# Optimization experiments

Measured on AMD Instinct MI355X. Metric: run time of the kernel, lower is better.

Reference implementation:

```python
import jax, jax.numpy as jnp
import numpy as np
import math

B, S, D, HD = 8, 2048, 768, 64  # batch, seq, emb_hidden_dim, head_dim


def setup_inputs() -> dict:
    key = jax.random.key(0)
    ks = jax.random.split(key, 7)
    scale_w = 1.0 / math.sqrt(D)
    return {
        "X": jax.random.normal(ks[0], (B, S, D), dtype=jnp.float32),
        "Wq": jax.random.normal(ks[1], (D, HD), dtype=jnp.float32) * scale_w,
        "bq": jax.random.normal(ks[2], (HD,), dtype=jnp.float32) * 0.01,
        "Wk": jax.random.normal(ks[3], (D, HD), dtype=jnp.float32) * scale_w,
        "bk": jax.random.normal(ks[4], (HD,), dtype=jnp.float32) * 0.01,
        "Wv": jax.random.normal(ks[5], (D, HD), dtype=jnp.float32) * scale_w,
        "bv": jax.random.normal(ks[6], (HD,), dtype=jnp.float32) * 0.01,
    }


def reference(X, Wq, bq, Wk, bk, Wv, bv):
    # Projections: [B,S,D] @ [D,HD] -> [B,S,HD]
    Q = X @ Wq + bq
    K = X @ Wk + bk
    V = X @ Wv + bv
    # NOTE: original divides by sqrt(hidden_dim)=sqrt(D), not sqrt(head_dim)
    inv_scale = 1.0 / math.sqrt(D)
    scores = jnp.einsum("bqd,bkd->bqk", Q, K) * inv_scale  # [B,S,S]
    causal = jnp.tril(jnp.ones((S, S), dtype=bool))
    scores = jnp.where(causal, scores, -jnp.inf)
    attn = jax.nn.softmax(scores, axis=-1)
    # dropout p=0.0 (eval/deterministic reference)
    return jnp.einsum("bqk,bkd->bqd", attn, V)  # [B,S,HD]
```

## Files before the change

kernel.cpp:

```cpp
#include <hip/hip_runtime.h>
#include <hip/hip_bf16.h>
#include <math.h>

typedef __attribute__((ext_vector_type(8))) short short8;
typedef __attribute__((ext_vector_type(4))) float f32x4;

#define SS 2048
#define DD 768
#define HDIM 64
#define MM 16384

__device__ __forceinline__ short f2bf(float f) {
    union { float f; unsigned u; } v; v.f = f;
    unsigned r = (v.u + 0x7fffu + ((v.u >> 16) & 1u)) >> 16;
    return (short)r;
}

__device__ __forceinline__ void gl_lds(const void* g, void* l) {
    __builtin_amdgcn_global_load_lds(
        (const __attribute__((address_space(1))) unsigned*)g,
        (__attribute__((address_space(3))) unsigned*)l, 16, 0, 0);
}

__global__ void prep_w(const float* __restrict__ Wq, const float* __restrict__ Wk,
                       const float* __restrict__ Wv, short* __restrict__ Wt) {
    int idx = blockIdx.x * 256 + threadIdx.x;
    int col = idx / DD;
    int k   = idx - col * DD;
    const float* W = (col < 64) ? Wq : (col < 128) ? Wk : Wv;
    int c = col & 63;
    Wt[idx] = f2bf(W[k * HDIM + c]);
}

__global__ __launch_bounds__(512)
void proj_qkv(const float* __restrict__ X, const short* __restrict__ Wt,
              const float* __restrict__ bq, const float* __restrict__ bk,
              const float* __restrict__ bv,
              short* __restrict__ Qg, short* __restrict__ Kg, short* __restrict__ Vt) {
    __shared__ float Xl[2][2048];
    __shared__ short Wl[2][12288];
    const int tid = threadIdx.x;
    const int w = tid >> 6, lane = tid & 63;
    const int lr = lane & 15, lg = lane >> 4;
    const int wr = w >> 2, wc = w & 3;
    const int row0 = blockIdx.x * 32;

    f32x4 acc[3];
    #pragma unroll
    for (int cf = 0; cf < 3; cf++) acc[cf] = (f32x4)0.0f;

    auto stage = [&](int kk, int buf) {
        {
            int o = w * 1024 + lane * 16;
            int row = o >> 8, ch = (o >> 4) & 15;
            const char* src = (const char*)X + (size_t)(row0 + row) * 3072
                              + kk * 256 + ((ch ^ (row & 7)) << 4);
            gl_lds(src, (char*)&Xl[buf][0] + w * 1024);
        }
        #pragma unroll
        for (int s = 0; s < 3; s++) {
            int i = w * 3 + s;
            int o = i * 1024 + lane * 16;
            int col = o >> 7, ch = (o >> 4) & 7;
            const char* src = (const char*)Wt + (size_t)col * 1536
                              + kk * 128 + ((ch ^ (col & 7)) << 4);
            gl_lds(src, (char*)&Wl[buf][0] + i * 1024);
        }
    };

    stage(0, 0);
    __syncthreads();
    int buf = 0;
    for (int kk = 0; kk < 12; kk++) {
        if (kk < 11) stage(kk + 1, buf ^ 1);
        const char* xb = (const char*)&Xl[buf][0];
        const char* wb = (const char*)&Wl[buf][0];
        #pragma unroll
        for (int ksub = 0; ksub < 2; ksub++) {
            int r = wr * 16 + lr;
            int b0 = r * 256 + ksub * 128 + lg * 32;
            f32x4 x0 = *(const f32x4*)(xb + ((b0)      ^ ((r & 7) << 4)));
            f32x4 x1 = *(const f32x4*)(xb + ((b0 + 16) ^ ((r & 7) << 4)));
            short8 a;
            a[0]=f2bf(x0[0]); a[1]=f2bf(x0[1]); a[2]=f2bf(x0[2]); a[3]=f2bf(x0[3]);
            a[4]=f2bf(x1[0]); a[5]=f2bf(x1[1]); a[6]=f2bf(x1[2]); a[7]=f2bf(x1[3]);
            #pragma unroll
            for (int cf = 0; cf < 3; cf++) {
                int col = wc * 48 + cf * 16 + lr;
                short8 bfr = *(const short8*)(wb +
                    ((col * 128 + ksub * 64 + lg * 16) ^ ((col & 7) << 4)));
                acc[cf] = __builtin_amdgcn_mfma_f32_16x16x32_bf16(a, bfr, acc[cf], 0, 0, 0);
            }
        }
        __syncthreads();
        buf ^= 1;
    }

    #pragma unroll
    for (int cf = 0; cf < 3; cf++) {
        int gcol = wc * 48 + cf * 16 + lr;
        int m = gcol >> 6, cc = gcol & 63;
        float bias = (m == 0 ? bq : m == 1 ? bk : bv)[cc];
        #pragma unroll
        for (int i = 0; i < 4; i++) {
            int r = row0 + wr * 16 + lg * 4 + i;
            short o = f2bf(acc[cf][i] + bias);
            if (m == 0)      Qg[(size_t)r * HDIM + cc] = o;
            else if (m == 1) Kg[(size_t)r * HDIM + cc] = o;
            else             Vt[(size_t)cc * MM + r]   = o;
        }
    }
}

__global__ __launch_bounds__(512)
void attn_part(const short* __restrict__ Qg, const short* __restrict__ Kg,
               const short* __restrict__ Vt,
               float* __restrict__ Opart, float* __restrict__ Ml) {
    __shared__ short Kl[2][4096];
    __shared__ short Vl[2][4096];
    __shared__ short Pl[8][1024];
    const int tid = threadIdx.x;
    const int w = tid >> 6, lane = tid & 63;
    const int lr = lane & 15, lg = lane >> 4;
    const int b = blockIdx.y;

    int idx = 39 - (int)blockIdx.x;
    int g = 0;
    while (idx >= 2 * (g + 1) * (g + 2)) g++;
    int rem = idx - 2 * g * (g + 1);
    const int J = g * 4 + rem / (g + 1);
    const int c = rem - (rem / (g + 1)) * (g + 1);
    const int t0 = c * 8;
    const int t1 = min(2 * J + 2, t0 + 8);

    const int q0 = J * 128 + w * 16;
    char* plbase = (char*)&Pl[w][0];

    short8 qf[2];
    qf[0] = *(const short8*)(Qg + ((size_t)b * SS + q0 + lr) * HDIM + lg * 8);
    qf[1] = *(const short8*)(Qg + ((size_t)b * SS + q0 + lr) * HDIM + 32 + lg * 8);

    f32x4 oacc[4];
    #pragma unroll
    for (int d = 0; d < 4; d++) oacc[d] = (f32x4)0.0f;
    float mrow[4] = {-INFINITY, -INFINITY, -INFINITY, -INFINITY};
    float lrow[4] = {0.f, 0.f, 0.f, 0.f};
    const float scl = 0.03608439182435161f;

    auto stage = [&](int t, int buf) {
        const int kv0 = t * 64;
        {
            int o = w * 1024 + lane * 16;
            int row = o >> 7, ch = (o >> 4) & 7;
            const char* src = (const char*)Kg + ((size_t)b * SS + kv0) * 128
                              + row * 128 + ((ch ^ (row & 7)) << 4);
            gl_lds(src, (char*)&Kl[buf][0] + w * 1024);
        }
        {
            int o = w * 1024 + lane * 16;
            int col = o >> 7, ch = (o >> 4) & 7;
            const char* src = (const char*)Vt + (size_t)col * (MM * 2)
                              + ((size_t)b * SS + kv0) * 2 + ((ch ^ (col & 7)) << 4);
            gl_lds(src, (char*)&Vl[buf][0] + w * 1024);
        }
    };

    stage(t0, 0);
    __syncthreads();
    int buf = 0;
    for (int t = t0; t < t1; t++) {
        if (t + 1 < t1) stage(t + 1, buf ^ 1);
        const int kv0 = t * 64;
        const bool active = (kv0 <= q0 + 15);
        if (active) {
            const char* kb = (const char*)&Kl[buf][0];
            f32x4 sacc[4];
            #pragma unroll
            for (int ct = 0; ct < 4; ct++) sacc[ct] = (f32x4)0.0f;
            #pragma unroll
            for (int ct = 0; ct < 4; ct++) {
                int row = ct * 16 + lr;
                short8 k0 = *(const short8*)(kb + ((row * 128 +      lg * 16) ^ ((row & 7) << 4)));
                short8 k1 = *(const short8*)(kb + ((row * 128 + 64 + lg * 16) ^ ((row & 7) << 4)));
                sacc[ct] = __builtin_amdgcn_mfma_f32_16x16x32_bf16(qf[0], k0, sacc[ct], 0, 0, 0);
                sacc[ct] = __builtin_amdgcn_mfma_f32_16x16x32_bf16(qf[1], k1, sacc[ct], 0, 0, 0);
            }

            const bool maskt = (kv0 + 63 > q0);
            float p[4][4];
            float rm[4] = {-1e30f, -1e30f, -1e30f, -1e30f};
            #pragma unroll
            for (int ct = 0; ct < 4; ct++) {
                #pragma unroll
                for (int i = 0; i < 4; i++) {
                    float s = sacc[ct][i] * scl;
                    if (maskt) {
                        int kv = kv0 + ct * 16 + lr;
                        int qr = q0 + lg * 4 + i;
                        if (kv > qr) s = -1e30f;
                    }
                    p[ct][i] = s;
                    rm[i] = fmaxf(rm[i], s);
                }
            }
            #pragma unroll
            for (int i = 0; i < 4; i++) {
                float v = rm[i];
                v = fmaxf(v, __shfl_xor(v, 1));
                v = fmaxf(v, __shfl_xor(v, 2));
                v = fmaxf(v, __shfl_xor(v, 4));
                v = fmaxf(v, __shfl_xor(v, 8));
                rm[i] = v;
            }
            float rs[4];
            #pragma unroll
            for (int i = 0; i < 4; i++) {
                float mn = fmaxf(mrow[i], rm[i]);
                float scale = __expf(mrow[i] - mn);
                mrow[i] = mn;
                lrow[i] *= scale;
                for (int d = 0; d < 4; d++) oacc[d][i] *= scale;
                float sum = 0.f;
                #pragma unroll
                for (int ct = 0; ct < 4; ct++) {
                    float e = __expf(p[ct][i] - mn);
                    p[ct][i] = e;
                    sum += e;
                }
                rs[i] = sum;
            }
            #pragma unroll
            for (int i = 0; i < 4; i++) {
                float v = rs[i];
                v += __shfl_xor(v, 1);
                v += __shfl_xor(v, 2);
                v += __shfl_xor(v, 4);
                v += __shfl_xor(v, 8);
                lrow[i] += v;
            }

            #pragma unroll
            for (int ct = 0; ct < 4; ct++) {
                #pragma unroll
                for (int i = 0; i < 4; i++) {
                    int r = lg * 4 + i;
                    int byteoff = r * 128 + (ct * 16 + lr) * 2;
                    *(short*)(plbase + (byteoff ^ ((r & 7) << 4))) = f2bf(p[ct][i]);
                }
            }

            const char* vb = (const char*)&Vl[buf][0];
            #pragma unroll
            for (int ks = 0; ks < 2; ks++) {
                int byteoff = lr * 128 + ks * 64 + lg * 16;
                short8 pf = *(const short8*)(plbase + (byteoff ^ ((lr & 7) << 4)));
                #pragma unroll
                for (int d = 0; d < 4; d++) {
                    int col = d * 16 + lr;
                    short8 vf = *(const short8*)(vb +
                        ((col * 128 + ks * 64 + lg * 16) ^ ((col & 7) << 4)));
                    oacc[d] = __builtin_amdgcn_mfma_f32_16x16x32_bf16(pf, vf, oacc[d], 0, 0, 0);
                }
            }
        }
        __syncthreads();
        buf ^= 1;
    }

    const int pb = (b * 16 + J) * 4 + c;
    float* op = Opart + (size_t)pb * 8192 + (size_t)(w * 16) * 64;
    #pragma unroll
    for (int d = 0; d < 4; d++)
        #pragma unroll
        for (int i = 0; i < 4; i++)
            op[(lg * 4 + i) * 64 + d * 16 + lr] = oacc[d][i];
    if (lr == 0) {
        float* ml = Ml + (size_t)pb * 256;
        for (int i = 0; i < 4; i++) {
            ml[w * 16 + lg * 4 + i]       = mrow[i];
            ml[128 + w * 16 + lg * 4 + i] = lrow[i];
        }
    }
}

__global__ __launch_bounds__(256)
void attn_comb(const float* __restrict__ Opart, const float* __restrict__ Ml,
               float* __restrict__ out) {
    const int J = blockIdx.x, b = blockIdx.y;
    const int nc = (2 * J + 2 + 7) >> 3;
    const int tid = threadIdx.x;
    const int r = tid >> 1, h = tid & 1;
    const int base = (b * 16 + J) * 4;

    float m = -INFINITY;
    for (int c = 0; c < nc; c++) m = fmaxf(m, Ml[(size_t)(base + c) * 256 + r]);

    float L = 0.f;
    f32x4 acc[8];
    #pragma unroll
    for (int q = 0; q < 8; q++) acc[q] = (f32x4)0.0f;
    for (int c = 0; c < nc; c++) {
        const float* ml = Ml + (size_t)(base + c) * 256;
        float sc = __expf(ml[r] - m);
        L += ml[128 + r] * sc;
        const float* op = Opart + (size_t)(base + c) * 8192 + r * 64 + h * 32;
        #pragma unroll
        for (int q = 0; q < 8; q++)
            acc[q] += *(const f32x4*)(op + q * 4) * sc;
    }
    float inv = 1.0f / L;
    float* o = out + ((size_t)b * SS + J * 128 + r) * HDIM + h * 32;
    #pragma unroll
    for (int q = 0; q < 8; q++) {
        f32x4 v = acc[q] * inv;
        *(f32x4*)(o + q * 4) = v;
    }
}

extern "C" void kernel_launch(void* const* d_in, const int* in_sizes, int n_in,
                              void* d_out, int out_size, void* d_ws, size_t ws_size,
                              hipStream_t stream) {
    const float* X  = (const float*)d_in[0];
    const float* Wq = (const float*)d_in[1];
    const float* bq = (const float*)d_in[2];
    const float* Wk = (const float*)d_in[3];
    const float* bk = (const float*)d_in[4];
    const float* Wv = (const float*)d_in[5];
    const float* bv = (const float*)d_in[6];
    float* out = (float*)d_out;

    char* ws = (char*)d_ws;
    short* Wt = (short*)(ws);
    short* Qg = (short*)(ws + 294912);
    short* Kg = (short*)(ws + 294912 + 2097152);
    short* Vt = (short*)(ws + 294912 + 2 * 2097152);
    size_t opOff = 294912 + 3 * (size_t)2097152;
    float* Op = (float*)(ws + opOff);
    float* Ml = (float*)(ws + opOff + (size_t)512 * 8192 * 4);

    prep_w<<<576, 256, 0, stream>>>(Wq, Wk, Wv, Wt);
    proj_qkv<<<512, 512, 0, stream>>>(X, Wt, bq, bk, bv, Qg, Kg, Vt);
    attn_part<<<dim3(40, 8), 512, 0, stream>>>(Qg, Kg, Vt, Op, Ml);
    attn_comb<<<dim3(16, 8), 256, 0, stream>>>(Op, Ml, out);
}
```

Baseline: 62.36 us.

## Skip masked MFMA sub-tiles, write single-chunk rows directly, store partials in bf16

On diagonal tiles the attention kernel now computes only the 16-column sub-tiles at or below the causal boundary, applies the mask only to the boundary sub-tile, and skips P·V k-steps that are entirely masked. Query blocks J<=3 have a single KV chunk, so they normalize and write the final output directly, and the combine kernel only handles J>=4. Partial outputs are stored as bf16 instead of fp32, halving the partial-buffer traffic at some cost in precision. The goal is to cut wasted matrix work, combine work and memory traffic, at the price of more branching and a small accuracy loss.

```diff
diff --git a/kernel.cpp b/kernel.cpp
--- a/kernel.cpp
+++ b/kernel.cpp
@@ -14,6 +14,11 @@
     union { float f; unsigned u; } v; v.f = f;
     unsigned r = (v.u + 0x7fffu + ((v.u >> 16) & 1u)) >> 16;
     return (short)r;
+}
+__device__ __forceinline__ float bf2f(short s) {
+    union { float f; unsigned u; } v;
+    v.u = ((unsigned)(unsigned short)s) << 16;
+    return v.f;
 }
 
 __device__ __forceinline__ void gl_lds(const void* g, void* l) {
@@ -115,7 +120,8 @@
 __global__ __launch_bounds__(512)
 void attn_part(const short* __restrict__ Qg, const short* __restrict__ Kg,
                const short* __restrict__ Vt,
-               float* __restrict__ Opart, float* __restrict__ Ml) {
+               short* __restrict__ Opart, float* __restrict__ Ml,
+               float* __restrict__ out) {
     __shared__ short Kl[2][4096];
     __shared__ short Vl[2][4096];
     __shared__ short Pl[8][1024];
@@ -128,7 +134,7 @@
     int g = 0;
     while (idx >= 2 * (g + 1) * (g + 2)) g++;
     int rem = idx - 2 * g * (g + 1);
-    const int J = g * 4 + rem / (g + 1);
+    const int J = 4 * g + rem / (g + 1);
     const int c = rem - (rem / (g + 1)) * (g + 1);
     const int t0 = c * 8;
     const int t1 = min(2 * J + 2, t0 + 8);
@@ -171,36 +177,43 @@
     for (int t = t0; t < t1; t++) {
         if (t + 1 < t1) stage(t + 1, buf ^ 1);
         const int kv0 = t * 64;
-        const bool active = (kv0 <= q0 + 15);
-        if (active) {
+        const int delta = q0 - kv0;
+        if (delta >= 0) {
+            const int nct = min(4, (delta >> 4) + 1);
+            const int mct = delta >> 4;
+            const int nks = min(2, (delta >> 5) + 1);
+
             const char* kb = (const char*)&Kl[buf][0];
             f32x4 sacc[4];
             #pragma unroll
-            for (int ct = 0; ct < 4; ct++) sacc[ct] = (f32x4)0.0f;
-            #pragma unroll
             for (int ct = 0; ct < 4; ct++) {
-                int row = ct * 16 + lr;
-                short8 k0 = *(const short8*)(kb + ((row * 128 +      lg * 16) ^ ((row & 7) << 4)));
-                short8 k1 = *(const short8*)(kb + ((row * 128 + 64 + lg * 16) ^ ((row & 7) << 4)));
-                sacc[ct] = __builtin_amdgcn_mfma_f32_16x16x32_bf16(qf[0], k0, sacc[ct], 0, 0, 0);
-                sacc[ct] = __builtin_amdgcn_mfma_f32_16x16x32_bf16(qf[1], k1, sacc[ct], 0, 0, 0);
-            }
-
-            const bool maskt = (kv0 + 63 > q0);
+                if (ct < nct) {
+                    int row = ct * 16 + lr;
+                    short8 k0 = *(const short8*)(kb + ((row * 128 +      lg * 16) ^ ((row & 7) << 4)));
+                    short8 k1 = *(const short8*)(kb + ((row * 128 + 64 + lg * 16) ^ ((row & 7) << 4)));
+                    f32x4 s = (f32x4)0.0f;
+                    s = __builtin_amdgcn_mfma_f32_16x16x32_bf16(qf[0], k0, s, 0, 0, 0);
+                    s = __builtin_amdgcn_mfma_f32_16x16x32_bf16(qf[1], k1, s, 0, 0, 0);
+                    sacc[ct] = s;
+                }
+            }
+
             float p[4][4];
             float rm[4] = {-1e30f, -1e30f, -1e30f, -1e30f};
             #pragma unroll
             for (int ct = 0; ct < 4; ct++) {
-                #pragma unroll
-                for (int i = 0; i < 4; i++) {
-                    float s = sacc[ct][i] * scl;
-                    if (maskt) {
-                        int kv = kv0 + ct * 16 + lr;
-                        int qr = q0 + lg * 4 + i;
-                        if (kv > qr) s = -1e30f;
+                if (ct < nct) {
+                    #pragma unroll
+                    for (int i = 0; i < 4; i++) {
+                        float s = sacc[ct][i] * scl;
+                        if (ct == mct) {
+                            int kv = kv0 + ct * 16 + lr;
+                            int qr = q0 + lg * 4 + i;
+                            if (kv > qr) s = -1e30f;
+                        }
+                        p[ct][i] = s;
+                        rm[i] = fmaxf(rm[i], s);
                     }
-                    p[ct][i] = s;
-                    rm[i] = fmaxf(rm[i], s);
                 }
             }
             #pragma unroll
@@ -223,9 +236,11 @@
                 float sum = 0.f;
                 #pragma unroll
                 for (int ct = 0; ct < 4; ct++) {
-                    float e = __expf(p[ct][i] - mn);
-                    p[ct][i] = e;
-                    sum += e;
+                    if (ct < nct) {
+                        float e = __expf(p[ct][i] - mn);
+                        p[ct][i] = e;
+                        sum += e;
+                    }
                 }
                 rs[i] = sum;
             }
@@ -241,25 +256,30 @@
 
             #pragma unroll
             for (int ct = 0; ct < 4; ct++) {
-                #pragma unroll
-                for (int i = 0; i < 4; i++) {
-                    int r = lg * 4 + i;
-                    int byteoff = r * 128 + (ct * 16 + lr) * 2;
-                    *(short*)(plbase + (byteoff ^ ((r & 7) << 4))) = f2bf(p[ct][i]);
+                if (ct < 2 * nks) {
+                    #pragma unroll
+                    for (int i = 0; i < 4; i++) {
+                        int r = lg * 4 + i;
+                        int byteoff = r * 128 + (ct * 16 + lr) * 2;
+                        short val = (ct < nct) ? f2bf(p[ct][i]) : (short)0;
+                        *(short*)(plbase + (byteoff ^ ((r & 7) << 4))) = val;
+                    }
                 }
             }
 
             const char* vb = (const char*)&Vl[buf][0];
             #pragma unroll
             for (int ks = 0; ks < 2; ks++) {
-                int byteoff = lr * 128 + ks * 64 + lg * 16;
-                short8 pf = *(const short8*)(plbase + (byteoff ^ ((lr & 7) << 4)));
-                #pragma unroll
-                for (int d = 0; d < 4; d++) {
-                    int col = d * 16 + lr;
-                    short8 vf = *(const short8*)(vb +
-                        ((col * 128 + ks * 64 + lg * 16) ^ ((col & 7) << 4)));
-                    oacc[d] = __builtin_amdgcn_mfma_f32_16x16x32_bf16(pf, vf, oacc[d], 0, 0, 0);
+                if (ks < nks) {
+                    int byteoff = lr * 128 + ks * 64 + lg * 16;
+                    short8 pf = *(const short8*)(plbase + (byteoff ^ ((lr & 7) << 4)));
+                    #pragma unroll
+                    for (int d = 0; d < 4; d++) {
+                        int col = d * 16 + lr;
+                        short8 vf = *(const short8*)(vb +
+                            ((col * 128 + ks * 64 + lg * 16) ^ ((col & 7) << 4)));
+                        oacc[d] = __builtin_amdgcn_mfma_f32_16x16x32_bf16(pf, vf, oacc[d], 0, 0, 0);
+                    }
                 }
             }
         }
@@ -267,27 +287,36 @@
         buf ^= 1;
     }
 
-    const int pb = (b * 16 + J) * 4 + c;
-    float* op = Opart + (size_t)pb * 8192 + (size_t)(w * 16) * 64;
-    #pragma unroll
-    for (int d = 0; d < 4; d++)
-        #pragma unroll
-        for (int i = 0; i < 4; i++)
-            op[(lg * 4 + i) * 64 + d * 16 + lr] = oacc[d][i];
-    if (lr == 0) {
-        float* ml = Ml + (size_t)pb * 256;
-        for (int i = 0; i < 4; i++) {
-            ml[w * 16 + lg * 4 + i]       = mrow[i];
-            ml[128 + w * 16 + lg * 4 + i] = lrow[i];
+    if (J <= 3) {
+        #pragma unroll
+        for (int d = 0; d < 4; d++)
+            #pragma unroll
+            for (int i = 0; i < 4; i++)
+                out[((size_t)b * SS + q0 + lg * 4 + i) * HDIM + d * 16 + lr]
+                    = oacc[d][i] / lrow[i];
+    } else {
+        const int pb = (b * 16 + J) * 4 + c;
+        short* op = Opart + (size_t)pb * 8192 + (size_t)(w * 16) * 64;
+        #pragma unroll
+        for (int d = 0; d < 4; d++)
+            #pragma unroll
+            for (int i = 0; i < 4; i++)
+                op[(lg * 4 + i) * 64 + d * 16 + lr] = f2bf(oacc[d][i]);
+        if (lr == 0) {
+            float* ml = Ml + (size_t)pb * 256;
+            for (int i = 0; i < 4; i++) {
+                ml[w * 16 + lg * 4 + i]       = mrow[i];
+                ml[128 + w * 16 + lg * 4 + i] = lrow[i];
+            }
         }
     }
 }
 
 __global__ __launch_bounds__(256)
-void attn_comb(const float* __restrict__ Opart, const float* __restrict__ Ml,
+void attn_comb(const short* __restrict__ Opart, const float* __restrict__ Ml,
                float* __restrict__ out) {
-    const int J = blockIdx.x, b = blockIdx.y;
-    const int nc = (2 * J + 2 + 7) >> 3;
+    const int J = blockIdx.x + 4, b = blockIdx.y;
+    const int nc = (J >> 2) + 1;
     const int tid = threadIdx.x;
     const int r = tid >> 1, h = tid & 1;
     const int base = (b * 16 + J) * 4;
@@ -303,10 +332,15 @@
         const float* ml = Ml + (size_t)(base + c) * 256;
         float sc = __expf(ml[r] - m);
         L += ml[128 + r] * sc;
-        const float* op = Opart + (size_t)(base + c) * 8192 + r * 64 + h * 32;
-        #pragma unroll
-        for (int q = 0; q < 8; q++)
-            acc[q] += *(const f32x4*)(op + q * 4) * sc;
+        const short* op = Opart + (size_t)(base + c) * 8192 + r * 64 + h * 32;
+        #pragma unroll
+        for (int q = 0; q < 4; q++) {
+            short8 s = *(const short8*)(op + q * 8);
+            f32x4 lo = {bf2f(s[0]), bf2f(s[1]), bf2f(s[2]), bf2f(s[3])};
+            f32x4 hi = {bf2f(s[4]), bf2f(s[5]), bf2f(s[6]), bf2f(s[7])};
+            acc[q * 2]     += lo * sc;
+            acc[q * 2 + 1] += hi * sc;
+        }
     }
     float inv = 1.0f / L;
     float* o = out + ((size_t)b * SS + J * 128 + r) * HDIM + h * 32;
@@ -335,11 +369,11 @@
     short* Kg = (short*)(ws + 294912 + 2097152);
     short* Vt = (short*)(ws + 294912 + 2 * 2097152);
     size_t opOff = 294912 + 3 * (size_t)2097152;
-    float* Op = (float*)(ws + opOff);
-    float* Ml = (float*)(ws + opOff + (size_t)512 * 8192 * 4);
+    short* Op = (short*)(ws + opOff);
+    float* Ml = (float*)(ws + opOff + (size_t)512 * 8192 * 2);
 
     prep_w<<<576, 256, 0, stream>>>(Wq, Wk, Wv, Wt);
     proj_qkv<<<512, 512, 0, stream>>>(X, Wt, bq, bk, bv, Qg, Kg, Vt);
-    attn_part<<<dim3(40, 8), 512, 0, stream>>>(Qg, Kg, Vt, Op, Ml);
-    attn_comb<<<dim3(16, 8), 256, 0, stream>>>(Op, Ml, out);
-}
+    attn_part<<<dim3(40, 8), 512, 0, stream>>>(Qg, Kg, Vt, Op, Ml, out);
+    attn_comb<<<dim3(12, 8), 256, 0, stream>>>(Op, Ml, out);
+}
```

New measurement: 75.43 us. +20.9%, slower.
